# Kernel optimization log

Measured on AMD Instinct MI355X. Metric: run time of the kernel, lower is better.

## Reference

```python
import jax, jax.numpy as jnp
import numpy as np

TEMPERATURE = 0.07
BASE_TEMPERATURE = 0.07


def setup_inputs() -> dict:
    key = jax.random.key(0)
    k1, k2 = jax.random.split(key)
    feat1 = jax.random.normal(k1, (4096, 128), dtype=jnp.float32)
    feat2 = jax.random.normal(k2, (4096, 128), dtype=jnp.float32)
    return {"feat1": feat1, "feat2": feat2}


def reference(feat1, feat2):
    # world_size = 1 -> gather is identity; N = per-gpu batch size
    N = feat1.shape[0]
    two_n = 2 * N
    features = jnp.concatenate([feat1, feat2], axis=0)          # [2N, C]
    # F.normalize(dim=1)
    norm = jnp.linalg.norm(features, axis=1, keepdims=True)
    features = features / jnp.maximum(norm, 1e-12)
    logits = jnp.matmul(features, features.T) / TEMPERATURE      # [2N, 2N]
    logits = logits - jax.lax.stop_gradient(
        jnp.max(logits, axis=1, keepdims=True))
    # neg_mask = ~eye: sum of exp over off-diagonal entries per row
    exp_sum = jnp.sum(jnp.exp(logits), axis=1) - jnp.exp(jnp.diagonal(logits))
    # pos_mask: row i pairs with column (i + N) mod 2N
    idx = jnp.arange(two_n)
    pos = logits[idx, (idx + N) % two_n]                          # [2N]
    log_prob = pos - jnp.log(exp_sum)
    loss = -(TEMPERATURE / BASE_TEMPERATURE) * jnp.mean(log_prob)
    return loss
```

## Files before the change

kernel.cpp:

```cpp
#include <hip/hip_runtime.h>

typedef unsigned short u16;
typedef __attribute__((ext_vector_type(8))) short short8;
typedef __attribute__((ext_vector_type(4))) float f32x4;

#define INVT 14.285714285714286f
#define KEXP 20.617062471830945f

__device__ __forceinline__ u16 f2bf(float f) {
  union { float f; unsigned u; } v; v.f = f;
  unsigned u = v.u;
  u += 0x7fffu + ((u >> 16) & 1u);
  return (u16)(u >> 16);
}
__device__ __forceinline__ float bf2f(u16 h) {
  union { unsigned u; float f; } v; v.u = ((unsigned)h) << 16;
  return v.f;
}
__device__ __forceinline__ void glds16(const u16* g, u16* l) {
  __builtin_amdgcn_global_load_lds((const __attribute__((address_space(1))) void*)g,
                                   (__attribute__((address_space(3))) void*)l,
                                   16, 0, 0);
}

__global__ __launch_bounds__(256) void norm_kernel(
    const float* __restrict__ f1, const float* __restrict__ f2,
    u16* __restrict__ F, float* __restrict__ dvec, float* __restrict__ pos,
    float* __restrict__ accum, int* __restrict__ done, int N) {
  const int b = blockIdx.x, tid = threadIdx.x;
  const int wave = tid >> 6, l = tid & 63;
  if (b == 0 && tid == 0) { *accum = 0.0f; *done = 0; }
#pragma unroll
  for (int it = 0; it < 2; ++it) {
    int i = b * 8 + wave * 2 + it;
    if (i >= N) break;
    const float* a = f1 + (size_t)i * 128;
    const float* c = f2 + (size_t)i * 128;
    float a0 = a[l], a1 = a[l + 64];
    float b0 = c[l], b1 = c[l + 64];
    float sa = a0 * a0 + a1 * a1;
    float sb = b0 * b0 + b1 * b1;
#pragma unroll
    for (int o = 32; o; o >>= 1) { sa += __shfl_xor(sa, o); sb += __shfl_xor(sb, o); }
    float ia = 1.0f / fmaxf(sqrtf(sa), 1e-12f);
    float ib = 1.0f / fmaxf(sqrtf(sb), 1e-12f);
    u16 ba0 = f2bf(a0 * ia), ba1 = f2bf(a1 * ia);
    u16 bb0 = f2bf(b0 * ib), bb1 = f2bf(b1 * ib);
    u16* Fa = F + (size_t)i * 128;
    u16* Fb = F + (size_t)(i + N) * 128;
    Fa[l] = ba0; Fa[l + 64] = ba1;
    Fb[l] = bb0; Fb[l + 64] = bb1;
    float fa0 = bf2f(ba0), fa1 = bf2f(ba1);
    float fb0 = bf2f(bb0), fb1 = bf2f(bb1);
    float s1 = fa0 * fa0 + fa1 * fa1;
    float s2 = fb0 * fb0 + fb1 * fb1;
    float cr = fa0 * fb0 + fa1 * fb1;
#pragma unroll
    for (int o = 32; o; o >>= 1) {
      s1 += __shfl_xor(s1, o); s2 += __shfl_xor(s2, o); cr += __shfl_xor(cr, o);
    }
    if (l == 0) {
      dvec[i]     = exp2f(fmaf(s1, KEXP, -KEXP));
      dvec[i + N] = exp2f(fmaf(s2, KEXP, -KEXP));
      pos[i] = cr;
      pos[i + N] = cr;
    }
  }
}

__global__ __launch_bounds__(256, 2) void gemm_exp_kernel(
    const u16* __restrict__ F, float* __restrict__ P, int TWO_N) {
  __shared__ __align__(16) u16 At[128 * 128];
  __shared__ __align__(16) u16 Bt[128 * 128];
  __shared__ float colsum[128];
  __shared__ float rowsum[128];
  const int tid = threadIdx.x;
  const int wave = tid >> 6, lane = tid & 63;
  int p = blockIdx.x;
  int bj = (int)((sqrtf(8.0f * (float)p + 1.0f) - 1.0f) * 0.5f);
  while ((bj + 1) * (bj + 2) / 2 <= p) ++bj;
  while (bj * (bj + 1) / 2 > p) --bj;
  const int bi = p - bj * (bj + 1) / 2;
  const bool diag = (bi == bj);

  if (tid < 128) { colsum[tid] = 0.0f; rowsum[tid] = 0.0f; }
  {
    const u16* Bb = F + (size_t)bj * (128 * 128);
#pragma unroll
    for (int t = 0; t < 8; ++t) {
      int chunk = wave * 8 + t;
      int g = chunk * 64 + lane;
      int gg = g ^ ((g >> 4) & 7);
      glds16(Bb + (size_t)gg * 8, &Bt[chunk * 512]);
    }
  }
  if (!diag) {
    const u16* Ab = F + (size_t)bi * (128 * 128);
#pragma unroll
    for (int t = 0; t < 8; ++t) {
      int chunk = wave * 8 + t;
      int g = chunk * 64 + lane;
      int gg = g ^ ((g >> 4) & 7);
      glds16(Ab + (size_t)gg * 8, &At[chunk * 512]);
    }
  }
  __syncthreads();

  const int wr = wave >> 1, wc = wave & 1;
  const int q = lane >> 4, m = lane & 15;
  const u16* asrc = diag ? Bt : At;
  f32x4 acc[4][4];
#pragma unroll
  for (int fr = 0; fr < 4; ++fr)
#pragma unroll
    for (int cf = 0; cf < 4; ++cf) acc[fr][cf] = (f32x4)(0.0f);

#pragma unroll
  for (int ks = 0; ks < 4; ++ks) {
    const int c = ks * 4 + q;
    short8 av[4], bv[4];
#pragma unroll
    for (int fr = 0; fr < 4; ++fr) {
      int rr = wr * 64 + fr * 16 + m;
      av[fr] = *(const short8*)&asrc[rr * 128 + ((c ^ (rr & 7)) * 8)];
    }
#pragma unroll
    for (int cf = 0; cf < 4; ++cf) {
      int rr = wc * 64 + cf * 16 + m;
      bv[cf] = *(const short8*)&Bt[rr * 128 + ((c ^ (rr & 7)) * 8)];
    }
#pragma unroll
    for (int fr = 0; fr < 4; ++fr)
#pragma unroll
      for (int cf = 0; cf < 4; ++cf)
        acc[fr][cf] = __builtin_amdgcn_mfma_f32_16x16x32_bf16(av[fr], bv[cf], acc[fr][cf], 0, 0, 0);
  }

  float cs[4] = {0.f, 0.f, 0.f, 0.f};
  float v[16];
#pragma unroll
  for (int i = 0; i < 16; ++i) v[i] = 0.f;
#pragma unroll
  for (int cf = 0; cf < 4; ++cf)
#pragma unroll
    for (int fr = 0; fr < 4; ++fr)
#pragma unroll
      for (int rg = 0; rg < 4; ++rg) {
        float e = exp2f(fmaf(acc[fr][cf][rg], KEXP, -KEXP));
        cs[cf] += e;
        v[fr * 4 + rg] += e;
      }
#pragma unroll
  for (int cf = 0; cf < 4; ++cf) {
    cs[cf] += __shfl_xor(cs[cf], 16);
    cs[cf] += __shfl_xor(cs[cf], 32);
    if (q == 0) atomicAdd(&colsum[wc * 64 + cf * 16 + m], cs[cf]);
  }
  if (!diag) {
    float t16[16];
#pragma unroll
    for (int i = 0; i < 16; ++i) t16[i] = __shfl_xor(v[i], 8);
    bool hi = (m & 8) != 0;
#pragma unroll
    for (int i = 0; i < 8; ++i) v[i] = hi ? (v[i + 8] + t16[i + 8]) : (v[i] + t16[i]);
#pragma unroll
    for (int i = 0; i < 8; ++i) t16[i] = __shfl_xor(v[i], 4);
    hi = (m & 4) != 0;
#pragma unroll
    for (int i = 0; i < 4; ++i) v[i] = hi ? (v[i + 4] + t16[i + 4]) : (v[i] + t16[i]);
#pragma unroll
    for (int i = 0; i < 4; ++i) t16[i] = __shfl_xor(v[i], 2);
    hi = (m & 2) != 0;
#pragma unroll
    for (int i = 0; i < 2; ++i) v[i] = hi ? (v[i + 2] + t16[i + 2]) : (v[i] + t16[i]);
    t16[0] = __shfl_xor(v[0], 1);
    t16[1] = __shfl_xor(v[1], 1);
    v[0] = (m & 1) ? (v[1] + t16[1]) : (v[0] + t16[0]);
    atomicAdd(&rowsum[wr * 64 + (m >> 2) * 16 + q * 4 + (m & 3)], v[0]);
  }
  __syncthreads();
  if (tid < 128) {
    P[(size_t)bi * TWO_N + bj * 128 + tid] = colsum[tid];
    if (!diag) P[(size_t)bj * TWO_N + bi * 128 + tid] = rowsum[tid];
  }
}

__global__ __launch_bounds__(256) void reduce_kernel(
    const float* __restrict__ P, const float* __restrict__ dvec,
    const float* __restrict__ pos, float* __restrict__ accum,
    int* __restrict__ done, float* __restrict__ out, int TWO_N, int NB) {
  __shared__ float wpart[4];
  __shared__ int ticket_s;
  const int tid = threadIdx.x;
  const int wave = tid >> 6, lane = tid & 63;
  const int j = blockIdx.x * 256 + tid;
  float e = 0.0f;
#pragma unroll 8
  for (int o = 0; o < NB; ++o) e += P[(size_t)o * TWO_N + j];
  float term = (pos[j] - 1.0f) * INVT - logf(e - dvec[j]);
#pragma unroll
  for (int o = 32; o; o >>= 1) term += __shfl_xor(term, o);
  if (lane == 0) wpart[wave] = term;
  __syncthreads();
  if (tid == 0) {
    atomicAdd(accum, wpart[0] + wpart[1] + wpart[2] + wpart[3]);
    __threadfence();
    ticket_s = atomicAdd(done, 1);
    if (ticket_s == gridDim.x - 1) {
      float tot = atomicAdd(accum, 0.0f);
      out[0] = tot * (-1.0f / (float)TWO_N);
    }
  }
}

extern "C" void kernel_launch(void* const* d_in, const int* in_sizes, int n_in,
                              void* d_out, int out_size, void* d_ws, size_t ws_size,
                              hipStream_t stream) {
  const float* f1 = (const float*)d_in[0];
  const float* f2 = (const float*)d_in[1];
  int N = in_sizes[0] / 128;
  int TWO_N = 2 * N;
  int NB = TWO_N / 128;
  int NT = NB * (NB + 1) / 2;

  char* ws = (char*)d_ws;
  u16*   F     = (u16*)ws;
  float* dvec  = (float*)(ws + (size_t)TWO_N * 128 * 2);
  float* pos   = dvec + TWO_N;
  float* P     = pos + TWO_N;
  float* accum = P + (size_t)NB * TWO_N;
  int*   done  = (int*)(accum + 1);

  norm_kernel<<<512, 256, 0, stream>>>(f1, f2, F, dvec, pos, accum, done, N);
  gemm_exp_kernel<<<NT, 256, 0, stream>>>(F, P, TWO_N);
  reduce_kernel<<<TWO_N / 256, 256, 0, stream>>>(P, dvec, pos, accum, done,
                                                 (float*)d_out, TWO_N, NB);
}
```

Measured before the change: 92.02 us.

## Fuse row normalization into GEMM tile loads and derive diag/pos from MFMA accumulators

Removes the separate normalization kernel. Each GEMM block now loads its fp32 rows directly, normalizes them, converts to bf16 and writes swizzled tiles into LDS. The diagonal exp terms and positive-pair logits are taken from the MFMA accumulators on diagonal tiles and on the tiles offset by N. This saves one launch and the bf16 workspace round trip, but every tile recomputes normalization and reads twice as many bytes of fp32 input. The direct global_load_lds async path is replaced by register loads.

```diff
diff --git a/kernel.cpp b/kernel.cpp
--- a/kernel.cpp
+++ b/kernel.cpp
@@ -13,63 +13,11 @@
   u += 0x7fffu + ((u >> 16) & 1u);
   return (u16)(u >> 16);
 }
-__device__ __forceinline__ float bf2f(u16 h) {
-  union { unsigned u; float f; } v; v.u = ((unsigned)h) << 16;
-  return v.f;
-}
-__device__ __forceinline__ void glds16(const u16* g, u16* l) {
-  __builtin_amdgcn_global_load_lds((const __attribute__((address_space(1))) void*)g,
-                                   (__attribute__((address_space(3))) void*)l,
-                                   16, 0, 0);
-}
-
-__global__ __launch_bounds__(256) void norm_kernel(
+
+__global__ __launch_bounds__(256, 2) void gemm_exp_kernel(
     const float* __restrict__ f1, const float* __restrict__ f2,
-    u16* __restrict__ F, float* __restrict__ dvec, float* __restrict__ pos,
-    float* __restrict__ accum, int* __restrict__ done, int N) {
-  const int b = blockIdx.x, tid = threadIdx.x;
-  const int wave = tid >> 6, l = tid & 63;
-  if (b == 0 && tid == 0) { *accum = 0.0f; *done = 0; }
-#pragma unroll
-  for (int it = 0; it < 2; ++it) {
-    int i = b * 8 + wave * 2 + it;
-    if (i >= N) break;
-    const float* a = f1 + (size_t)i * 128;
-    const float* c = f2 + (size_t)i * 128;
-    float a0 = a[l], a1 = a[l + 64];
-    float b0 = c[l], b1 = c[l + 64];
-    float sa = a0 * a0 + a1 * a1;
-    float sb = b0 * b0 + b1 * b1;
-#pragma unroll
-    for (int o = 32; o; o >>= 1) { sa += __shfl_xor(sa, o); sb += __shfl_xor(sb, o); }
-    float ia = 1.0f / fmaxf(sqrtf(sa), 1e-12f);
-    float ib = 1.0f / fmaxf(sqrtf(sb), 1e-12f);
-    u16 ba0 = f2bf(a0 * ia), ba1 = f2bf(a1 * ia);
-    u16 bb0 = f2bf(b0 * ib), bb1 = f2bf(b1 * ib);
-    u16* Fa = F + (size_t)i * 128;
-    u16* Fb = F + (size_t)(i + N) * 128;
-    Fa[l] = ba0; Fa[l + 64] = ba1;
-    Fb[l] = bb0; Fb[l + 64] = bb1;
-    float fa0 = bf2f(ba0), fa1 = bf2f(ba1);
-    float fb0 = bf2f(bb0), fb1 = bf2f(bb1);
-    float s1 = fa0 * fa0 + fa1 * fa1;
-    float s2 = fb0 * fb0 + fb1 * fb1;
-    float cr = fa0 * fb0 + fa1 * fb1;
-#pragma unroll
-    for (int o = 32; o; o >>= 1) {
-      s1 += __shfl_xor(s1, o); s2 += __shfl_xor(s2, o); cr += __shfl_xor(cr, o);
-    }
-    if (l == 0) {
-      dvec[i]     = exp2f(fmaf(s1, KEXP, -KEXP));
-      dvec[i + N] = exp2f(fmaf(s2, KEXP, -KEXP));
-      pos[i] = cr;
-      pos[i + N] = cr;
-    }
-  }
-}
-
-__global__ __launch_bounds__(256, 2) void gemm_exp_kernel(
-    const u16* __restrict__ F, float* __restrict__ P, int TWO_N) {
+    float* __restrict__ P, float* __restrict__ dvec, float* __restrict__ pos,
+    float* __restrict__ accum, int* __restrict__ done, int N, int TWO_N) {
   __shared__ __align__(16) u16 At[128 * 128];
   __shared__ __align__(16) u16 Bt[128 * 128];
   __shared__ float colsum[128];
@@ -77,6 +25,7 @@
   const int tid = threadIdx.x;
   const int wave = tid >> 6, lane = tid & 63;
   int p = blockIdx.x;
+  if (p == 0 && tid == 0) { *accum = 0.0f; *done = 0; }
   int bj = (int)((sqrtf(8.0f * (float)p + 1.0f) - 1.0f) * 0.5f);
   while ((bj + 1) * (bj + 2) / 2 <= p) ++bj;
   while (bj * (bj + 1) / 2 > p) --bj;
@@ -84,24 +33,35 @@
   const bool diag = (bi == bj);
 
   if (tid < 128) { colsum[tid] = 0.0f; rowsum[tid] = 0.0f; }
-  {
-    const u16* Bb = F + (size_t)bj * (128 * 128);
-#pragma unroll
-    for (int t = 0; t < 8; ++t) {
-      int chunk = wave * 8 + t;
-      int g = chunk * 64 + lane;
-      int gg = g ^ ((g >> 4) & 7);
-      glds16(Bb + (size_t)gg * 8, &Bt[chunk * 512]);
-    }
-  }
-  if (!diag) {
-    const u16* Ab = F + (size_t)bi * (128 * 128);
-#pragma unroll
-    for (int t = 0; t < 8; ++t) {
-      int chunk = wave * 8 + t;
-      int g = chunk * 64 + lane;
-      int gg = g ^ ((g >> 4) & 7);
-      glds16(Ab + (size_t)gg * 8, &At[chunk * 512]);
+
+  const int r = tid >> 1, h = tid & 1;
+#pragma unroll
+  for (int s = 0; s < 2; ++s) {
+    if (s == 0 && diag) continue;
+    const int rb = s ? bj : bi;
+    const int g = rb * 128 + r;
+    const float* src = (g < N) ? (f1 + (size_t)g * 128) : (f2 + (size_t)(g - N) * 128);
+    const float4* s4 = (const float4*)src + h * 16;
+    float4 v[16];
+    float ss = 0.0f;
+#pragma unroll
+    for (int k = 0; k < 16; ++k) {
+      v[k] = s4[k];
+      ss += v[k].x * v[k].x + v[k].y * v[k].y + v[k].z * v[k].z + v[k].w * v[k].w;
+    }
+    ss += __shfl_xor(ss, 1);
+    const float inv = 1.0f / fmaxf(sqrtf(ss), 1e-12f);
+    u16* dst = s ? Bt : At;
+#pragma unroll
+    for (int k = 0; k < 8; ++k) {
+      float4 a = v[2 * k], b = v[2 * k + 1];
+      short8 gr;
+      gr[0] = (short)f2bf(a.x * inv); gr[1] = (short)f2bf(a.y * inv);
+      gr[2] = (short)f2bf(a.z * inv); gr[3] = (short)f2bf(a.w * inv);
+      gr[4] = (short)f2bf(b.x * inv); gr[5] = (short)f2bf(b.y * inv);
+      gr[6] = (short)f2bf(b.z * inv); gr[7] = (short)f2bf(b.w * inv);
+      const int gc = (h * 8 + k) ^ (r & 7);
+      *(short8*)&dst[(r * 16 + gc) * 8] = gr;
     }
   }
   __syncthreads();
@@ -134,6 +94,24 @@
 #pragma unroll
       for (int cf = 0; cf < 4; ++cf)
         acc[fr][cf] = __builtin_amdgcn_mfma_f32_16x16x32_bf16(av[fr], bv[cf], acc[fr][cf], 0, 0, 0);
+  }
+
+  const bool dlane = (q == (m >> 2)) && (wr == wc);
+  if (diag && dlane) {
+#pragma unroll
+    for (int fr = 0; fr < 4; ++fr) {
+      float sv = acc[fr][fr][m & 3];
+      dvec[bj * 128 + wr * 64 + fr * 16 + m] = exp2f(fmaf(sv, KEXP, -KEXP));
+    }
+  }
+  if ((bj - bi) * 256 == TWO_N && dlane) {
+#pragma unroll
+    for (int fr = 0; fr < 4; ++fr) {
+      float sv = acc[fr][fr][m & 3];
+      int a = bi * 128 + wr * 64 + fr * 16 + m;
+      pos[a] = sv;
+      pos[a + N] = sv;
+    }
   }
 
   float cs[4] = {0.f, 0.f, 0.f, 0.f};
@@ -224,15 +202,14 @@
   int NT = NB * (NB + 1) / 2;
 
   char* ws = (char*)d_ws;
-  u16*   F     = (u16*)ws;
-  float* dvec  = (float*)(ws + (size_t)TWO_N * 128 * 2);
+  float* P     = (float*)ws;
+  float* dvec  = P + (size_t)NB * TWO_N;
   float* pos   = dvec + TWO_N;
-  float* P     = pos + TWO_N;
-  float* accum = P + (size_t)NB * TWO_N;
+  float* accum = pos + TWO_N;
   int*   done  = (int*)(accum + 1);
 
-  norm_kernel<<<512, 256, 0, stream>>>(f1, f2, F, dvec, pos, accum, done, N);
-  gemm_exp_kernel<<<NT, 256, 0, stream>>>(F, P, TWO_N);
+  gemm_exp_kernel<<<NT, 256, 0, stream>>>(f1, f2, P, dvec, pos, accum, done,
+                                          N, TWO_N);
   reduce_kernel<<<TWO_N / 256, 256, 0, stream>>>(P, dvec, pos, accum, done,
                                                  (float*)d_out, TWO_N, NB);
 }
```

New measurement: 110.4 us. 1.2x slower.
